# Kernel optimization log

Measured on AMD Instinct MI355X. Metric: run time of the kernel, lower is better.

The kernel has to match this reference:

```python
import jax, jax.numpy as jnp
import numpy as np

N_NODES = 100000
N_EDGES = 1600000
IN_C = 128
HID = 128
OUT_C = 10
N_GRAPHS = 512


def setup_inputs() -> dict:
    key = jax.random.key(0)
    ks = jax.random.split(key, 12)
    x = jax.random.normal(ks[0], (N_NODES, IN_C), dtype=jnp.float32)
    edge_index = jax.random.randint(ks[1], (2, N_EDGES), 0, N_NODES, dtype=jnp.int64)
    batch = jnp.sort(jax.random.randint(ks[2], (N_NODES,), 0, N_GRAPHS, dtype=jnp.int64))

    def lin(k, fan_in, fan_out):
        bound = 1.0 / np.sqrt(fan_in)
        return jax.random.uniform(k, (fan_in, fan_out), jnp.float32, -bound, bound)

    params = {
        # GraphConv layer i: W_rel (neighbor aggregate transform, with bias),
        # W_root (self transform, no bias) -- matches PyG GraphConv.
        "W1_rel": lin(ks[3], IN_C, HID), "b1": jnp.zeros((HID,), jnp.float32), "W1_root": lin(ks[4], IN_C, HID),
        "W2_rel": lin(ks[5], HID, HID), "b2": jnp.zeros((HID,), jnp.float32), "W2_root": lin(ks[6], HID, HID),
        "W3_rel": lin(ks[7], HID, HID), "b3": jnp.zeros((HID,), jnp.float32), "W3_root": lin(ks[8], HID, HID),
        "W_lin": lin(ks[9], HID, OUT_C), "b_lin": jnp.zeros((OUT_C,), jnp.float32),
    }
    return {"x": x, "edge_index": edge_index, "batch": batch, **params}


def _graph_conv(x, src, dst, W_rel, b, W_root):
    # PyG GraphConv with aggr='add': out_i = W_rel @ sum_{j->i} x_j + b + W_root @ x_i
    agg = jax.ops.segment_sum(x[src], dst, num_segments=x.shape[0])  # [N, d]
    return agg @ W_rel + b + x @ W_root


def reference(x, edge_index, batch,
              W1_rel, b1, W1_root,
              W2_rel, b2, W2_root,
              W3_rel, b3, W3_root,
              W_lin, b_lin):
    src, dst = edge_index[0], edge_index[1]
    h = jax.nn.relu(_graph_conv(x, src, dst, W1_rel, b1, W1_root))
    h = jax.nn.relu(_graph_conv(h, src, dst, W2_rel, b2, W2_root))
    h = _graph_conv(h, src, dst, W3_rel, b3, W3_root)
    # global mean pool over graphs
    sums = jax.ops.segment_sum(h, batch, num_segments=N_GRAPHS)             # [G, d]
    counts = jax.ops.segment_sum(jnp.ones((h.shape[0],), h.dtype), batch, num_segments=N_GRAPHS)
    pooled = sums / jnp.maximum(counts, 1.0)[:, None]
    return pooled @ W_lin + b_lin  # [G, OUT_C]
```

## Files before the change

kernel.cpp:

```cpp
#include <hip/hip_runtime.h>

static constexpr int NN = 100000;
static constexpr int NE = 1600000;
static constexpr int C  = 128;
static constexpr int OC = 10;
static constexpr int NG = 512;

static constexpr int BSH  = 9;
static constexpr int BNW  = 1 << BSH;
static constexpr int BK   = (NN + BNW - 1) / BNW;
static constexpr int BCAP = 12288;
static constexpr int EPB  = 8192;
static constexpr int ABLK = (NE + EPB - 1) / EPB;

static constexpr int TSTRIDE = 132;

typedef unsigned short u16;
typedef __attribute__((ext_vector_type(8))) short short8;
typedef __attribute__((ext_vector_type(8))) short bf16x8;
typedef __attribute__((ext_vector_type(4))) float f32x4;

__device__ __forceinline__ float bf2f(u16 u) {
    union { float f; unsigned int u32; } v; v.u32 = ((unsigned int)u) << 16; return v.f;
}
__device__ __forceinline__ u16 f2bf(float f) {
    union { float f; unsigned int u; } v; v.f = f;
    unsigned int u = v.u;
    unsigned int r = u + 0x7FFF + ((u >> 16) & 1);
    return (u16)(r >> 16);
}

__global__ __launch_bounds__(256) void k_binA(const int* __restrict__ src,
                                              const int* __restrict__ dst,
                                              int* __restrict__ gcnt,
                                              int* __restrict__ buck) {
    __shared__ int cnt[BK];
    __shared__ int curs[BK];
    int tid = threadIdx.x;
    for (int i = tid; i < BK; i += 256) cnt[i] = 0;
    __syncthreads();
    int e0 = blockIdx.x * EPB;
    for (int i = tid; i < EPB; i += 256) {
        int e = e0 + i;
        if (e < NE) atomicAdd(&cnt[dst[e] >> BSH], 1);
    }
    __syncthreads();
    for (int i = tid; i < BK; i += 256) {
        int c = cnt[i];
        int gb = (c > 0) ? atomicAdd(&gcnt[i], c) : 0;
        curs[i] = i * BCAP + gb;
    }
    __syncthreads();
    for (int i = tid; i < EPB; i += 256) {
        int e = e0 + i;
        if (e < NE) {
            int d = dst[e];
            int b = d >> BSH;
            int p = atomicAdd(&curs[b], 1);
            if (p < (b + 1) * BCAP)
                buck[p] = (src[e] << BSH) | (d & (BNW - 1));
        }
    }
}

__global__ __launch_bounds__(256) void k_meta(const int* __restrict__ gcnt,
                                              int* __restrict__ csrbase,
                                              int* __restrict__ rp,
                                              const int* __restrict__ batch,
                                              int* __restrict__ gstart) {
    int tid = threadIdx.x;
    if (blockIdx.x == 0) {
        __shared__ int buf[256];
        int v = (tid < BK) ? gcnt[tid] : 0;
        buf[tid] = v;
        __syncthreads();
        for (int off = 1; off < 256; off <<= 1) {
            int t = (tid >= off) ? buf[tid - off] : 0;
            __syncthreads();
            buf[tid] += t;
            __syncthreads();
        }
        if (tid < BK) csrbase[tid] = buf[tid] - v;
        if (tid == 0) rp[NN] = NE;
    } else {
        int g = (blockIdx.x - 1) * 256 + tid;
        if (g > NG) return;
        int lo = 0, hi = NN;
        while (lo < hi) { int mid = (lo + hi) >> 1; if (batch[mid] < g) lo = mid + 1; else hi = mid; }
        gstart[g] = lo;
    }
}

__global__ __launch_bounds__(BNW) void k_binB(const int* __restrict__ gcnt,
                                              const int* __restrict__ csrbase,
                                              const int* __restrict__ buck,
                                              int* __restrict__ rp,
                                              int* __restrict__ csr) {
    int b = blockIdx.x;
    int tid = threadIdx.x;
    __shared__ int hist[BNW];
    __shared__ int scanbuf[BNW];
    int n = gcnt[b];
    if (n > BCAP) n = BCAP;
    int base = csrbase[b];
    const int* bb = buck + (size_t)b * BCAP;

    hist[tid] = 0;
    __syncthreads();
    for (int i = tid; i < n; i += BNW) atomicAdd(&hist[bb[i] & (BNW - 1)], 1);
    __syncthreads();

    int v = hist[tid];
    scanbuf[tid] = v;
    __syncthreads();
    for (int off = 1; off < BNW; off <<= 1) {
        int t = (tid >= off) ? scanbuf[tid - off] : 0;
        __syncthreads();
        scanbuf[tid] += t;
        __syncthreads();
    }
    int excl = scanbuf[tid] - v;
    int node = (b << BSH) + tid;
    if (node < NN) rp[node] = base + excl;
    __syncthreads();
    hist[tid] = base + excl;
    __syncthreads();
    for (int i = tid; i < n; i += BNW) {
        int en = bb[i];
        int p = atomicAdd(&hist[en & (BNW - 1)], 1);
        csr[p] = en >> BSH;
    }
}

__global__ __launch_bounds__(256) void k_prep(
    const float* __restrict__ x, u16* __restrict__ xb,
    const float* __restrict__ W1r, const float* __restrict__ W1o,
    const float* __restrict__ W2r, const float* __restrict__ W2o,
    const float* __restrict__ W3r, const float* __restrict__ W3o,
    u16* __restrict__ Bp) {
    int bid = blockIdx.x;
    if (bid < 48) {
        int layer = bid >> 4;
        const float* Wr = (layer == 0) ? W1r : (layer == 1) ? W2r : W3r;
        const float* Wo = (layer == 0) ? W1o : (layer == 1) ? W2o : W3o;
        u16* out = Bp + layer * 32768;
        int t = (bid & 15) * 256 + threadIdx.x;
        int lane = t & 63;
        int nfrag = (t >> 6) & 7;
        int kk = t >> 9;
        int col = nfrag * 16 + (lane & 15);
        int k0 = kk * 32 + (lane >> 4) * 8;
        u16 vals[8];
#pragma unroll
        for (int j = 0; j < 8; ++j) {
            int k = k0 + j;
            float w = (k < C) ? Wr[k * C + col] : Wo[(k - C) * C + col];
            vals[j] = f2bf(w);
        }
        *reinterpret_cast<short8*>(out + (size_t)t * 8) = *reinterpret_cast<const short8*>(vals);
    } else {
        int i = (bid - 48) * 256 + threadIdx.x;
        size_t base = (size_t)i * 8;
        if (base >= (size_t)NN * C) return;
        float4 a = *reinterpret_cast<const float4*>(x + base);
        float4 b = *reinterpret_cast<const float4*>(x + base + 4);
        u16 o[8] = { f2bf(a.x), f2bf(a.y), f2bf(a.z), f2bf(a.w),
                     f2bf(b.x), f2bf(b.y), f2bf(b.z), f2bf(b.w) };
        *reinterpret_cast<short8*>(xb + base) = *reinterpret_cast<const short8*>(o);
    }
}

__global__ __launch_bounds__(256) void k_gather(const u16* __restrict__ h,
                                                const int* __restrict__ rp,
                                                const int* __restrict__ csr,
                                                u16* __restrict__ agg) {
    int t = blockIdx.x * blockDim.x + threadIdx.x;
    int node = t >> 6;
    if (node >= NN) return;
    int lane = t & 63;
    int jj = lane >> 4;
    int seg = (lane & 15) * 8;
    int beg = rp[node], end = rp[node + 1];

    float acc[8] = {};
    int j0 = beg;
    for (; j0 + 8 <= end; j0 += 8) {
        int sa = csr[j0 + jj];
        int sb = csr[j0 + 4 + jj];
        short8 va = *reinterpret_cast<const short8*>(h + (size_t)sa * C + seg);
        short8 vb = *reinterpret_cast<const short8*>(h + (size_t)sb * C + seg);
#pragma unroll
        for (int q = 0; q < 8; ++q) {
            acc[q] += bf2f((u16)va[q]);
            acc[q] += bf2f((u16)vb[q]);
        }
    }
    if (j0 < end) {
        int ja = j0 + jj;
        int jb = j0 + 4 + jj;
        if (ja < end) {
            int sa = csr[ja];
            short8 va = *reinterpret_cast<const short8*>(h + (size_t)sa * C + seg);
#pragma unroll
            for (int q = 0; q < 8; ++q) acc[q] += bf2f((u16)va[q]);
        }
        if (jb < end) {
            int sb = csr[jb];
            short8 vb = *reinterpret_cast<const short8*>(h + (size_t)sb * C + seg);
#pragma unroll
            for (int q = 0; q < 8; ++q) acc[q] += bf2f((u16)vb[q]);
        }
    }

#pragma unroll
    for (int q = 0; q < 8; ++q) {
        acc[q] += __shfl_xor(acc[q], 32);
        acc[q] += __shfl_xor(acc[q], 16);
    }
    if (lane < 16) {
        u16 o[8];
#pragma unroll
        for (int q = 0; q < 8; ++q) o[q] = f2bf(acc[q]);
        *reinterpret_cast<short8*>(agg + (size_t)node * C + seg) =
            *reinterpret_cast<const short8*>(o);
    }
}

template <bool RELU>
__global__ __launch_bounds__(256) void k_transform_mfma(
    const u16* __restrict__ agg, const u16* __restrict__ h,
    const u16* __restrict__ Bp, const float* __restrict__ bias,
    u16* __restrict__ out) {
    __shared__ u16 tile[4][16 * TSTRIDE];
    int wave = threadIdx.x >> 6;
    int lane = threadIdx.x & 63;
    int row0 = blockIdx.x * 64 + wave * 16;
    int arow = row0 + (lane & 15);
    int rclamp = arow < NN ? arow : NN - 1;
    int koff = (lane >> 4) * 8;

    f32x4 acc[8] = {};
#pragma unroll
    for (int kk = 0; kk < 8; ++kk) {
        bf16x8 a;
        if (kk < 4) {
            a = *reinterpret_cast<const bf16x8*>(agg + (size_t)rclamp * C + kk * 32 + koff);
        } else {
            a = *reinterpret_cast<const bf16x8*>(h + (size_t)rclamp * C + (kk - 4) * 32 + koff);
        }
        const u16* bp = Bp + ((size_t)kk * 8 * 64 + lane) * 8;
#pragma unroll
        for (int n = 0; n < 8; ++n) {
            bf16x8 b = *reinterpret_cast<const bf16x8*>(bp + (size_t)n * 64 * 8);
            acc[n] = __builtin_amdgcn_mfma_f32_16x16x32_bf16(a, b, acc[n], 0, 0, 0);
        }
    }

    u16* T = tile[wave];
    int colbase = lane & 15;
    int rloc = (lane >> 4) * 4;
#pragma unroll
    for (int n = 0; n < 8; ++n) {
        int col = n * 16 + colbase;
        float bb = bias[col];
#pragma unroll
        for (int r = 0; r < 4; ++r) {
            float v = acc[n][r] + bb;
            if (RELU) v = fmaxf(v, 0.0f);
            T[(rloc + r) * TSTRIDE + col] = f2bf(v);
        }
    }
    __syncthreads();

#pragma unroll
    for (int k = 0; k < 4; ++k) {
        int idx = k * 64 + lane;
        int lr = idx >> 4;
        int off = (idx & 15) * 8;
        int ro = row0 + lr;
        if (ro < NN) {
            short8 v = *reinterpret_cast<const short8*>(&T[lr * TSTRIDE + off]);
            *reinterpret_cast<short8*>(out + (size_t)ro * C + off) = v;
        }
    }
}

__global__ __launch_bounds__(256) void k_pool_final(
    const u16* __restrict__ h, const int* __restrict__ gstart,
    const float* __restrict__ W_lin, const float* __restrict__ b_lin,
    float* __restrict__ out) {
    int g = blockIdx.x;
    int rowslot = threadIdx.x >> 4;
    int seg = threadIdx.x & 15;
    int s = gstart[g], e = gstart[g + 1];

    float acc[8] = {};
    for (int i = s + rowslot; i < e; i += 16) {
        short8 v = *reinterpret_cast<const short8*>(h + (size_t)i * C + seg * 8);
#pragma unroll
        for (int q = 0; q < 8; ++q) acc[q] += bf2f((u16)v[q]);
    }

    __shared__ float red[16][C];
#pragma unroll
    for (int q = 0; q < 8; ++q) red[rowslot][seg * 8 + q] = acc[q];
    __syncthreads();

    __shared__ float sp[C];
    if (threadIdx.x < C) {
        float sum = 0.0f;
#pragma unroll
        for (int r = 0; r < 16; ++r) sum += red[r][threadIdx.x];
        float cnt = (float)max(e - s, 1);
        sp[threadIdx.x] = sum / cnt;
    }
    __syncthreads();
    if (threadIdx.x < OC) {
        float o = b_lin[threadIdx.x];
#pragma unroll 8
        for (int k = 0; k < C; ++k) o += sp[k] * W_lin[k * OC + threadIdx.x];
        out[g * OC + threadIdx.x] = o;
    }
}

extern "C" void kernel_launch(void* const* d_in, const int* in_sizes, int n_in,
                              void* d_out, int out_size, void* d_ws, size_t ws_size,
                              hipStream_t stream) {
    const float* x       = (const float*)d_in[0];
    const int*   eidx    = (const int*)d_in[1];
    const int*   batch   = (const int*)d_in[2];
    const float* W1_rel  = (const float*)d_in[3];
    const float* b1      = (const float*)d_in[4];
    const float* W1_root = (const float*)d_in[5];
    const float* W2_rel  = (const float*)d_in[6];
    const float* b2      = (const float*)d_in[7];
    const float* W2_root = (const float*)d_in[8];
    const float* W3_rel  = (const float*)d_in[9];
    const float* b3      = (const float*)d_in[10];
    const float* W3_root = (const float*)d_in[11];
    const float* W_lin   = (const float*)d_in[12];
    const float* b_lin   = (const float*)d_in[13];
    float* out = (float*)d_out;

    const int* src = eidx;
    const int* dst = eidx + NE;

    u16* xb   = (u16*)d_ws;
    u16* hb   = xb + (size_t)NN * C;
    u16* aggb = hb + (size_t)NN * C;
    u16* Bp   = aggb + (size_t)NN * C;
    int* rp      = (int*)(Bp + 3 * 32768);
    int* csr     = rp + NN + 1;
    int* buck    = csr + NE;
    int* gcnt    = buck + (size_t)BK * BCAP;
    int* csrbase = gcnt + BK;
    int* gstart  = csrbase + BK;

    const int gb = (NN * 64 + 255) / 256;
    const int tb = (NN + 63) / 64;
    const int prepb = 48 + ((NN * C / 8) + 255) / 256;

    hipMemsetAsync(gcnt, 0, BK * sizeof(int), stream);
    k_binA<<<ABLK, 256, 0, stream>>>(src, dst, gcnt, buck);
    k_meta<<<4, 256, 0, stream>>>(gcnt, csrbase, rp, batch, gstart);
    k_binB<<<BK, BNW, 0, stream>>>(gcnt, csrbase, buck, rp, csr);

    k_prep<<<prepb, 256, 0, stream>>>(x, xb, W1_rel, W1_root, W2_rel, W2_root,
                                      W3_rel, W3_root, Bp);

    k_gather<<<gb, 256, 0, stream>>>(xb, rp, csr, aggb);
    k_transform_mfma<true><<<tb, 256, 0, stream>>>(aggb, xb, Bp, b1, hb);

    k_gather<<<gb, 256, 0, stream>>>(hb, rp, csr, aggb);
    k_transform_mfma<true><<<tb, 256, 0, stream>>>(aggb, hb, Bp + 32768, b2, hb);

    k_gather<<<gb, 256, 0, stream>>>(hb, rp, csr, aggb);
    k_transform_mfma<false><<<tb, 256, 0, stream>>>(aggb, hb, Bp + 2 * 32768, b3, hb);

    k_pool_final<<<NG, 256, 0, stream>>>(hb, gstart, W_lin, b_lin, out);
}
```

Measured before the change: 335.0 us.

## Fold third GraphConv layer into mean pooling and the final linear

Layer 3 has no nonlinearity, and mean pooling plus the output linear are linear too. The change therefore replaces the third gather and MFMA transform with per-graph sums. Edges whose destination lies in a graph are summed from the dst-sorted CSR, and node features are summed per graph in a separate accumulator. W3_rel, W3_root and b3 are pre-multiplied with W_lin in a tiny kernel, so the per-graph output is a pair of 128x10 products. This removes the aggregate write/read and one dense transform pass, at the cost of an extra edge-wise gather into per-graph split partials.

```diff
diff --git a/kernel.cpp b/kernel.cpp
--- a/kernel.cpp
+++ b/kernel.cpp
@@ -14,6 +14,7 @@
 static constexpr int ABLK = (NE + EPB - 1) / EPB;
 
 static constexpr int TSTRIDE = 132;
+static constexpr int NSPLIT = 8;
 
 typedef unsigned short u16;
 typedef __attribute__((ext_vector_type(8))) short short8;
@@ -136,13 +137,12 @@
     const float* __restrict__ x, u16* __restrict__ xb,
     const float* __restrict__ W1r, const float* __restrict__ W1o,
     const float* __restrict__ W2r, const float* __restrict__ W2o,
-    const float* __restrict__ W3r, const float* __restrict__ W3o,
     u16* __restrict__ Bp) {
     int bid = blockIdx.x;
-    if (bid < 48) {
+    if (bid < 32) {
         int layer = bid >> 4;
-        const float* Wr = (layer == 0) ? W1r : (layer == 1) ? W2r : W3r;
-        const float* Wo = (layer == 0) ? W1o : (layer == 1) ? W2o : W3o;
+        const float* Wr = (layer == 0) ? W1r : W2r;
+        const float* Wo = (layer == 0) ? W1o : W2o;
         u16* out = Bp + layer * 32768;
         int t = (bid & 15) * 256 + threadIdx.x;
         int lane = t & 63;
@@ -159,7 +159,7 @@
         }
         *reinterpret_cast<short8*>(out + (size_t)t * 8) = *reinterpret_cast<const short8*>(vals);
     } else {
-        int i = (bid - 48) * 256 + threadIdx.x;
+        int i = (bid - 32) * 256 + threadIdx.x;
         size_t base = (size_t)i * 8;
         if (base >= (size_t)NN * C) return;
         float4 a = *reinterpret_cast<const float4*>(x + base);
@@ -167,6 +167,32 @@
         u16 o[8] = { f2bf(a.x), f2bf(a.y), f2bf(a.z), f2bf(a.w),
                      f2bf(b.x), f2bf(b.y), f2bf(b.z), f2bf(b.w) };
         *reinterpret_cast<short8*>(xb + base) = *reinterpret_cast<const short8*>(o);
+    }
+}
+
+__global__ __launch_bounds__(256) void k_wfold(
+    const float* __restrict__ W3r, const float* __restrict__ W3o,
+    const float* __restrict__ b3, const float* __restrict__ W_lin,
+    const float* __restrict__ b_lin,
+    float* __restrict__ Wrl, float* __restrict__ Wro, float* __restrict__ bfold) {
+    int o = blockIdx.x;
+    int tid = threadIdx.x;
+    if (tid < 128) {
+        float s = 0.0f;
+#pragma unroll 8
+        for (int c = 0; c < C; ++c) s += W3r[tid * C + c] * W_lin[c * OC + o];
+        Wrl[tid * OC + o] = s;
+    } else {
+        int k = tid - 128;
+        float s = 0.0f;
+#pragma unroll 8
+        for (int c = 0; c < C; ++c) s += W3o[k * C + c] * W_lin[c * OC + o];
+        Wro[k * OC + o] = s;
+    }
+    if (tid == 0) {
+        float s = 0.0f;
+        for (int c = 0; c < C; ++c) s += b3[c] * W_lin[c * OC + o];
+        bfold[o] = b_lin[o] + s;
     }
 }
 
@@ -285,41 +311,98 @@
     }
 }
 
-__global__ __launch_bounds__(256) void k_pool_final(
-    const u16* __restrict__ h, const int* __restrict__ gstart,
-    const float* __restrict__ W_lin, const float* __restrict__ b_lin,
-    float* __restrict__ out) {
+__global__ __launch_bounds__(256) void k_gsum(
+    const u16* __restrict__ h, const int* __restrict__ rp,
+    const int* __restrict__ csr, const int* __restrict__ gstart,
+    float* __restrict__ partial) {
+    int b = blockIdx.x;
+    int g = b >> 3;
+    int p = b & 7;
+    int slot = threadIdx.x >> 4;
+    int seg = (threadIdx.x & 15) * 8;
+
+    int gs = gstart[g], ge = gstart[g + 1];
+    int es = rp[gs], ee = rp[ge];
+    int m = ee - es;
+    int js = es + (int)(((long long)m * p) >> 3);
+    int je = es + (int)(((long long)m * (p + 1)) >> 3);
+    int nn = ge - gs;
+    int is = gs + (int)(((long long)nn * p) >> 3);
+    int ie = gs + (int)(((long long)nn * (p + 1)) >> 3);
+
+    float accS[8] = {};
+    int j = js + slot;
+    for (; j + 16 < je; j += 32) {
+        int r0 = csr[j];
+        int r1 = csr[j + 16];
+        short8 v0 = *reinterpret_cast<const short8*>(h + (size_t)r0 * C + seg);
+        short8 v1 = *reinterpret_cast<const short8*>(h + (size_t)r1 * C + seg);
+#pragma unroll
+        for (int q = 0; q < 8; ++q) {
+            accS[q] += bf2f((u16)v0[q]);
+            accS[q] += bf2f((u16)v1[q]);
+        }
+    }
+    if (j < je) {
+        int r0 = csr[j];
+        short8 v0 = *reinterpret_cast<const short8*>(h + (size_t)r0 * C + seg);
+#pragma unroll
+        for (int q = 0; q < 8; ++q) accS[q] += bf2f((u16)v0[q]);
+    }
+
+    float accT[8] = {};
+    for (int i = is + slot; i < ie; i += 16) {
+        short8 v = *reinterpret_cast<const short8*>(h + (size_t)i * C + seg);
+#pragma unroll
+        for (int q = 0; q < 8; ++q) accT[q] += bf2f((u16)v[q]);
+    }
+
+    __shared__ float red[16][C];
+#pragma unroll
+    for (int q = 0; q < 8; ++q) red[slot][seg + q] = accS[q];
+    __syncthreads();
+    if (threadIdx.x < C) {
+        float s = 0.0f;
+#pragma unroll
+        for (int r = 0; r < 16; ++r) s += red[r][threadIdx.x];
+        partial[(size_t)b * 256 + threadIdx.x] = s;
+    }
+    __syncthreads();
+#pragma unroll
+    for (int q = 0; q < 8; ++q) red[slot][seg + q] = accT[q];
+    __syncthreads();
+    if (threadIdx.x < C) {
+        float s = 0.0f;
+#pragma unroll
+        for (int r = 0; r < 16; ++r) s += red[r][threadIdx.x];
+        partial[(size_t)b * 256 + 128 + threadIdx.x] = s;
+    }
+}
+
+__global__ __launch_bounds__(128) void k_gout(
+    const float* __restrict__ partial, const int* __restrict__ gstart,
+    const float* __restrict__ Wrl, const float* __restrict__ Wro,
+    const float* __restrict__ bfold, float* __restrict__ out) {
     int g = blockIdx.x;
-    int rowslot = threadIdx.x >> 4;
-    int seg = threadIdx.x & 15;
-    int s = gstart[g], e = gstart[g + 1];
-
-    float acc[8] = {};
-    for (int i = s + rowslot; i < e; i += 16) {
-        short8 v = *reinterpret_cast<const short8*>(h + (size_t)i * C + seg * 8);
-#pragma unroll
-        for (int q = 0; q < 8; ++q) acc[q] += bf2f((u16)v[q]);
-    }
-
-    __shared__ float red[16][C];
-#pragma unroll
-    for (int q = 0; q < 8; ++q) red[rowslot][seg * 8 + q] = acc[q];
-    __syncthreads();
-
-    __shared__ float sp[C];
-    if (threadIdx.x < C) {
-        float sum = 0.0f;
-#pragma unroll
-        for (int r = 0; r < 16; ++r) sum += red[r][threadIdx.x];
-        float cnt = (float)max(e - s, 1);
-        sp[threadIdx.x] = sum / cnt;
-    }
-    __syncthreads();
-    if (threadIdx.x < OC) {
-        float o = b_lin[threadIdx.x];
+    int k = threadIdx.x;
+    __shared__ float S[C], T[C];
+    float s = 0.0f, t = 0.0f;
+#pragma unroll
+    for (int p = 0; p < NSPLIT; ++p) {
+        s += partial[((size_t)(g * NSPLIT + p)) * 256 + k];
+        t += partial[((size_t)(g * NSPLIT + p)) * 256 + 128 + k];
+    }
+    S[k] = s;
+    T[k] = t;
+    __syncthreads();
+    if (k < OC) {
+        int n = gstart[g + 1] - gstart[g];
+        float inv = 1.0f / (float)max(n, 1);
+        float o = bfold[k];
 #pragma unroll 8
-        for (int k = 0; k < C; ++k) o += sp[k] * W_lin[k * OC + threadIdx.x];
-        out[g * OC + threadIdx.x] = o;
+        for (int kk = 0; kk < C; ++kk)
+            o += (S[kk] * Wrl[kk * OC + k] + T[kk] * Wro[kk * OC + k]) * inv;
+        out[g * OC + k] = o;
     }
 }
 
@@ -349,24 +432,28 @@
     u16* hb   = xb + (size_t)NN * C;
     u16* aggb = hb + (size_t)NN * C;
     u16* Bp   = aggb + (size_t)NN * C;
-    int* rp      = (int*)(Bp + 3 * 32768);
+    int* rp      = (int*)(Bp + 2 * 32768);
     int* csr     = rp + NN + 1;
     int* buck    = csr + NE;
     int* gcnt    = buck + (size_t)BK * BCAP;
     int* csrbase = gcnt + BK;
     int* gstart  = csrbase + BK;
+    float* partial = (float*)(gstart + NG + 2);
+    float* Wrl   = partial + (size_t)NG * NSPLIT * 256;
+    float* Wro   = Wrl + C * OC;
+    float* bfold = Wro + C * OC;
 
     const int gb = (NN * 64 + 255) / 256;
     const int tb = (NN + 63) / 64;
-    const int prepb = 48 + ((NN * C / 8) + 255) / 256;
+    const int prepb = 32 + ((NN * C / 8) + 255) / 256;
 
     hipMemsetAsync(gcnt, 0, BK * sizeof(int), stream);
     k_binA<<<ABLK, 256, 0, stream>>>(src, dst, gcnt, buck);
     k_meta<<<4, 256, 0, stream>>>(gcnt, csrbase, rp, batch, gstart);
     k_binB<<<BK, BNW, 0, stream>>>(gcnt, csrbase, buck, rp, csr);
 
-    k_prep<<<prepb, 256, 0, stream>>>(x, xb, W1_rel, W1_root, W2_rel, W2_root,
-                                      W3_rel, W3_root, Bp);
+    k_prep<<<prepb, 256, 0, stream>>>(x, xb, W1_rel, W1_root, W2_rel, W2_root, Bp);
+    k_wfold<<<OC, 256, 0, stream>>>(W3_rel, W3_root, b3, W_lin, b_lin, Wrl, Wro, bfold);
 
     k_gather<<<gb, 256, 0, stream>>>(xb, rp, csr, aggb);
     k_transform_mfma<true><<<tb, 256, 0, stream>>>(aggb, xb, Bp, b1, hb);
@@ -374,8 +461,6 @@
     k_gather<<<gb, 256, 0, stream>>>(hb, rp, csr, aggb);
     k_transform_mfma<true><<<tb, 256, 0, stream>>>(aggb, hb, Bp + 32768, b2, hb);
 
-    k_gather<<<gb, 256, 0, stream>>>(hb, rp, csr, aggb);
-    k_transform_mfma<false><<<tb, 256, 0, stream>>>(aggb, hb, Bp + 2 * 32768, b3, hb);
-
-    k_pool_final<<<NG, 256, 0, stream>>>(hb, gstart, W_lin, b_lin, out);
-}
+    k_gsum<<<NG * NSPLIT, 256, 0, stream>>>(hb, rp, csr, gstart, partial);
+    k_gout<<<NG, 128, 0, stream>>>(partial, gstart, Wrl, Wro, bfold, out);
+}
```

Result: faster. 317.3 us (-5.3%).
